# Optimization experiments

Hardware: AMD Instinct MI355X
Metric: run time of the kernel (lower is better)

Reference implementation:

```python
import jax, jax.numpy as jnp
import numpy as np

L, D_IN, D_OUT, H = 4096, 512, 256, 4
HEAD = D_OUT // H  # 64


def setup_inputs() -> dict:
    key = jax.random.key(0)
    k1, k2, k3, k4, k5 = jax.random.split(key, 5)
    h = jax.random.normal(k1, (L, D_IN), dtype=jnp.float32)
    A = jax.random.randint(k2, (L, L), 0, 2, dtype=jnp.int32)
    W = jax.random.normal(k3, (D_OUT, D_IN), dtype=jnp.float32) * 0.05
    attn = jax.random.normal(k4, (H, 2 * HEAD), dtype=jnp.float32) * 0.05
    out_w = jax.random.normal(k5, (D_OUT, D_OUT), dtype=jnp.float32) * 0.05
    out_b = jnp.zeros((D_OUT,), dtype=jnp.float32)
    return {"h": h, "A": A, "W": W, "attn": attn, "out_w": out_w, "out_b": out_b}


def reference(h, A, W, attn, out_w, out_b):
    # h: (L, D_in), A: (L, L) in {0,1}
    Lq = h.shape[0]
    n_heads, two_d = attn.shape
    d = two_d // 2
    Wh = (h @ W.T).reshape(Lq, n_heads, d)  # (L, H, d)
    # Algebraic rewrite of concat-score: e_ij = a1.Wh_i + a2.Wh_j
    a1, a2 = attn[:, :d], attn[:, d:]
    s_i = jnp.einsum("lhd,hd->lh", Wh, a1)  # (L, H)
    s_j = jnp.einsum("lhd,hd->lh", Wh, a2)  # (L, H)
    e = jax.nn.leaky_relu(s_i[:, None, :] + s_j[None, :, :], negative_slope=0.2)  # (L, L, H)
    mask = (A > 0)[:, :, None]  # (L, L, 1)
    NEG = jnp.asarray(-1e30, e.dtype)
    e = jnp.where(mask, e, NEG)
    # stable masked softmax over j (axis=1); rows with no neighbors -> alpha = 0
    m = jnp.max(e, axis=1, keepdims=True)
    m = jnp.where(m > NEG / 2, m, 0.0)
    ex = jnp.where(mask, jnp.exp(e - m), 0.0)
    denom = jnp.sum(ex, axis=1, keepdims=True)
    alpha = ex / jnp.where(denom > 0, denom, 1.0)  # (L, L, H)
    # dropout is identity in eval mode
    out = jnp.einsum("ijh,jhd->ihd", alpha, Wh).reshape(Lq, n_heads * d)
    return out @ out_w.T + out_b
```

## Files before the change

kernel.cpp:

```cpp
#include <hip/hip_runtime.h>
#include <hip/hip_bf16.h>

#define L_    4096
#define DIN   512
#define DOUT  256
#define NH    4
#define HD    64
#define JW    128

typedef unsigned short u16;
typedef __attribute__((ext_vector_type(8))) short short8;
typedef __attribute__((ext_vector_type(4))) float floatx4;

__device__ __forceinline__ float bf2f(u16 u) {
  union { unsigned u32; float f; } v; v.u32 = ((unsigned)u) << 16; return v.f;
}
__device__ __forceinline__ u16 f2bf(float f) {
  union { float f; unsigned u; } v; v.f = f;
  unsigned r = v.u + 0x7fff + ((v.u >> 16) & 1);
  return (u16)(r >> 16);
}
__device__ __forceinline__ unsigned cvt2(float a, float b) {
  __hip_bfloat162 v = __float22bfloat162_rn(make_float2(a, b));
  return *reinterpret_cast<unsigned*>(&v);
}
__device__ __forceinline__ short8 pack8(const float* __restrict__ p) {
  float4 a = *(const float4*)p, b = *(const float4*)(p + 4);
  union { unsigned u[4]; short8 s; } r;
  r.u[0] = cvt2(a.x, a.y); r.u[1] = cvt2(a.z, a.w);
  r.u[2] = cvt2(b.x, b.y); r.u[3] = cvt2(b.z, b.w);
  return r.s;
}

__device__ __forceinline__ void mfma_cdmap(int lane, int* rowm, int* colm) {
  const int c0 = lane & 15;
  union { u16 u[8]; short8 s; } a1, b1, a2, b2;
  const u16 one = f2bf(1.f), cid = f2bf((float)c0);
  #pragma unroll
  for (int j = 0; j < 8; ++j) { a1.u[j] = cid; b1.u[j] = one; a2.u[j] = one; b2.u[j] = cid; }
  floatx4 z = {0.f, 0.f, 0.f, 0.f};
  floatx4 dr = __builtin_amdgcn_mfma_f32_16x16x32_bf16(a1.s, b1.s, z, 0, 0, 0);
  floatx4 dc = __builtin_amdgcn_mfma_f32_16x16x32_bf16(a2.s, b2.s, z, 0, 0, 0);
  #pragma unroll
  for (int r = 0; r < 4; ++r) {
    rowm[r] = (int)(dr[r] * 0.03125f + 0.5f);
    colm[r] = (int)(dc[r] * 0.03125f + 0.5f);
  }
}

__global__ __launch_bounds__(256) void k_ab(const int* __restrict__ A,
                                            unsigned* __restrict__ Abits) {
  const int g = blockIdx.x * 256 + threadIdx.x;
  const int lane = threadIdx.x & 63;
  #pragma unroll
  for (int r = 0; r < 8; ++r) {
    const size_t gi = (size_t)r * 524288 + g;
    int4 v = *(const int4*)(A + gi * 4);
    unsigned nib = (v.x > 0 ? 1u : 0u) | (v.y > 0 ? 2u : 0u)
                 | (v.z > 0 ? 4u : 0u) | (v.w > 0 ? 8u : 0u);
    unsigned part = nib << ((lane & 7) * 4);
    part |= __shfl_xor(part, 1, 64);
    part |= __shfl_xor(part, 2, 64);
    part |= __shfl_xor(part, 4, 64);
    if ((lane & 7) == 0) Abits[gi >> 3] = part;
  }
}

__global__ __launch_bounds__(256) void k0b_wf(const float* __restrict__ W,
                                              u16* __restrict__ Wf) {
  const int g = blockIdx.x * 256 + threadIdx.x;
  const int col = g >> 4, kblock = g & 15;
  const int cg = col >> 6, nt = (col >> 4) & 3, c0 = col & 15;
  const float* src = W + (size_t)col * DIN + kblock * 32;
  u16* dst = Wf + ((size_t)(cg * 4 + nt) * 16 + kblock) * 512 + c0 * 8;
  #pragma unroll
  for (int q = 0; q < 4; ++q) {
    short8 v = pack8(src + q * 8);
    *(short8*)(dst + q * 128) = v;
  }
}

__global__ __launch_bounds__(1024) void k1_wh(
    const float* __restrict__ h, const u16* __restrict__ Wf,
    const float* __restrict__ attn,
    u16* __restrict__ WhTf, float* __restrict__ s1g, float2* __restrict__ bdg)
{
  const int i0 = blockIdx.x * 16;
  const int t = threadIdx.x;
  const int wv = t >> 6, lane = t & 63, q = lane >> 4, c0 = lane & 15;
  const int cg = wv & 3, kc = wv >> 2;
  int rowm[4], colm[4];
  mfma_cdmap(lane, rowm, colm);

  __shared__ u16  hT[16][DIN + 8];
  __shared__ float pA[16][DOUT + 8];
  __shared__ float pB[16][DOUT + 8];
  __shared__ float attnL[NH * 128];

  if (t < 512) attnL[t] = attn[t];
  {
    const int row = t >> 6, c8 = (t & 63) * 8;
    const float* hp = h + (size_t)(i0 + row) * DIN + c8;
    float4 a = *(const float4*)hp;
    float4 b = *(const float4*)(hp + 4);
    union { unsigned u[4]; int4 v; } pk;
    pk.u[0] = cvt2(a.x, a.y); pk.u[1] = cvt2(a.z, a.w);
    pk.u[2] = cvt2(b.x, b.y); pk.u[3] = cvt2(b.z, b.w);
    *(int4*)&hT[row][c8] = pk.v;
  }
  __syncthreads();

  floatx4 acc[4] = {};
  #pragma unroll
  for (int ktl = 0; ktl < 4; ++ktl) {
    const int kb = kc * 128 + ktl * 32 + q * 8;
    short8 af = *(const short8*)&hT[c0][kb];
    #pragma unroll
    for (int nt = 0; nt < 4; ++nt) {
      short8 bf = *(const short8*)(Wf + ((size_t)(cg * 4 + nt) * 16 + kc * 4 + ktl) * 512 + lane * 8);
      acc[nt] = __builtin_amdgcn_mfma_f32_16x16x32_bf16(af, bf, acc[nt], 0, 0, 0);
    }
  }

  auto writeT = [&](float (*P)[DOUT + 8]) {
    #pragma unroll
    for (int nt = 0; nt < 4; ++nt)
      #pragma unroll
      for (int r = 0; r < 4; ++r)
        P[rowm[r]][cg * 64 + nt * 16 + colm[r]] = acc[nt][r];
  };
  auto addB2A = [&]() {
    const int row = t >> 6, c4 = (t & 63) * 4;
    float4* a = (float4*)&pA[row][c4];
    float4 bv = *(float4*)&pB[row][c4];
    float4 av = *a;
    av.x += bv.x; av.y += bv.y; av.z += bv.z; av.w += bv.w;
    *a = av;
  };

  if (kc == 0) writeT(pA);
  if (kc == 1) writeT(pB);
  __syncthreads();
  addB2A();
  __syncthreads();
  if (kc == 2) writeT(pB);
  __syncthreads();
  addB2A();
  __syncthreads();
  if (kc == 3) writeT(pB);
  __syncthreads();
  addB2A();
  __syncthreads();

  if (t < 64) {
    const int r = t & 15, hh = t >> 4;
    float s1 = 0.f, s2 = 0.f;
    for (int d = 0; d < HD; ++d) {
      float v = pA[r][hh * 64 + d];
      s1 += v * attnL[hh * 128 + d];
      s2 += v * attnL[hh * 128 + 64 + d];
    }
    s1g[hh * L_ + i0 + r] = s1;
    bdg[hh * L_ + i0 + r] = make_float2(__expf(s2), __expf(0.2f * s2));
  }

  if (t < 256) {
    const int d = t;
    const int hd = d >> 6, nt = (d >> 4) & 3, dc0 = d & 15;
    const int jblock = i0 >> 5, qbase = (i0 & 31) >> 3;
    u16* base = WhTf + ((size_t)(hd * 4 + nt) * JW + jblock) * 512 + dc0 * 8;
    #pragma unroll
    for (int jh = 0; jh < 2; ++jh) {
      const int i = jh * 8;
      union { unsigned u[4]; int4 v; } pk;
      pk.u[0] = cvt2(pA[i + 0][d], pA[i + 1][d]);
      pk.u[1] = cvt2(pA[i + 2][d], pA[i + 3][d]);
      pk.u[2] = cvt2(pA[i + 4][d], pA[i + 5][d]);
      pk.u[3] = cvt2(pA[i + 6][d], pA[i + 7][d]);
      *(int4*)(base + (qbase + jh) * 128) = pk.v;
    }
  }
}

__global__ __launch_bounds__(1024) void k2_attn(
    const unsigned* __restrict__ Abits, const u16* __restrict__ WhTf,
    const float* __restrict__ s1g, const float2* __restrict__ bdg,
    const float* __restrict__ out_w, const float* __restrict__ out_b,
    float* __restrict__ out)
{
  const int i0 = blockIdx.x * 16;
  const int t = threadIdx.x;
  const int wv = t >> 6, lane = t & 63, q = lane >> 4, c0 = lane & 15;
  const int hd = wv & 3, jc = wv >> 2;

  __shared__ float pA[NH][16][HD + 4];
  __shared__ float pB[NH][16][HD + 4];
  __shared__ float dden[NH][4][16];
  __shared__ float rcpS[NH][16];
  __shared__ u16  CnL[16][DOUT + 8];
  __shared__ unsigned AbitL[16][JW + 2];

  {
    const int row = t >> 6, l = t & 63;
    uint2 w2 = *(const uint2*)&Abits[(size_t)(i0 + row) * JW + l * 2];
    AbitL[row][l * 2] = w2.x;
    AbitL[row][l * 2 + 1] = w2.y;
  }
  int rowm[4], colm[4];
  mfma_cdmap(lane, rowm, colm);
  __syncthreads();

  const float s1v = s1g[hd * L_ + i0 + c0];
  const float av = __expf(s1v);
  const float cv = __expf(0.2f * s1v);
  const float th = __expf(-s1v);
  const float2* bdh = bdg + (size_t)hd * L_;
  const u16* Wc = WhTf + (size_t)(hd * 4) * JW * 512 + (size_t)(jc * 32) * 512 + lane * 8;
  const int jbase = jc * 1024;

  floatx4 acc[4] = {};
  float dpart = 0.f;

  union PF { unsigned u[4]; short8 s; };

  auto issueV = [&](int kt, float4* v) {
    const float2* p = bdh + jbase + kt * 32 + q * 8;
    v[0] = *(const float4*)p;       v[1] = *(const float4*)(p + 2);
    v[2] = *(const float4*)(p + 4); v[3] = *(const float4*)(p + 6);
  };
  auto issueW = [&](int kt, short8* w) {
    #pragma unroll
    for (int nt = 0; nt < 4; ++nt)
      w[nt] = *(const short8*)(Wc + ((size_t)nt * JW + kt) * 512);
  };
  auto sm8 = [&](const float4* v, int kt, PF& pf) {
    const unsigned mb = (AbitL[c0][jc * 32 + kt] >> (q * 8)) & 0xffu;
    const float bb[8] = {v[0].x, v[0].z, v[1].x, v[1].z, v[2].x, v[2].z, v[3].x, v[3].z};
    const float dd[8] = {v[0].y, v[0].w, v[1].y, v[1].w, v[2].y, v[2].w, v[3].y, v[3].w};
    float ex[8];
    #pragma unroll
    for (int jj = 0; jj < 8; ++jj) {
      float p = (bb[jj] >= th) ? (av * bb[jj]) : (cv * dd[jj]);
      ex[jj] = ((mb >> jj) & 1u) ? p : 0.f;
      dpart += ex[jj];
    }
    pf.u[0] = cvt2(ex[0], ex[1]); pf.u[1] = cvt2(ex[2], ex[3]);
    pf.u[2] = cvt2(ex[4], ex[5]); pf.u[3] = cvt2(ex[6], ex[7]);
  };
  auto mfma4 = [&](PF& pf, const short8* w) {
    #pragma unroll
    for (int nt = 0; nt < 4; ++nt)
      acc[nt] = __builtin_amdgcn_mfma_f32_16x16x32_bf16(pf.s, w[nt], acc[nt], 0, 0, 0);
  };

  float4 vA[4], vB[4];
  short8 wA[4], wB[4];
  PF pfA, pfB;

  issueV(0, vA); issueW(0, wA);
  issueV(1, vB); issueW(1, wB);
  __builtin_amdgcn_sched_barrier(0);
  sm8(vA, 0, pfA);

  #pragma unroll 1
  for (int u = 0; u < 15; ++u) {
    const int kt = 2 * u;
    issueV(kt + 2, vA);
    __builtin_amdgcn_sched_barrier(0);
    sm8(vB, kt + 1, pfB);
    mfma4(pfA, wA);
    __builtin_amdgcn_sched_barrier(0);
    issueW(kt + 2, wA);
    issueV(kt + 3, vB);
    __builtin_amdgcn_sched_barrier(0);
    mfma4(pfB, wB);
    __builtin_amdgcn_sched_barrier(0);
    issueW(kt + 3, wB);
    sm8(vA, kt + 2, pfA);
    __builtin_amdgcn_sched_barrier(0);
  }
  mfma4(pfA, wA);
  sm8(vB, 31, pfB);
  mfma4(pfB, wB);

  dpart += __shfl_xor(dpart, 16, 64);
  dpart += __shfl_xor(dpart, 32, 64);
  if (lane < 16) dden[hd][jc][lane] = dpart;

  auto writeT = [&](float (*P)[HD + 4]) {
    #pragma unroll
    for (int nt = 0; nt < 4; ++nt)
      #pragma unroll
      for (int r = 0; r < 4; ++r)
        P[rowm[r]][nt * 16 + colm[r]] = acc[nt][r];
  };
  auto addB2A = [&]() {
    const int h2 = t >> 8, rem = t & 255, row = rem >> 4, d4 = (rem & 15) * 4;
    float4* a = (float4*)&pA[h2][row][d4];
    float4 bv = *(float4*)&pB[h2][row][d4];
    float4 av2 = *a;
    av2.x += bv.x; av2.y += bv.y; av2.z += bv.z; av2.w += bv.w;
    *a = av2;
  };

  if (jc == 0) writeT(pA[hd]);
  if (jc == 1) writeT(pB[hd]);
  __syncthreads();
  if (t < 64) {
    const int hh = t >> 4, r = t & 15;
    float den = dden[hh][0][r] + dden[hh][1][r] + dden[hh][2][r] + dden[hh][3][r];
    rcpS[hh][r] = (den > 0.f) ? (1.f / den) : 0.f;
  }
  addB2A();
  __syncthreads();
  if (jc == 2) writeT(pB[hd]);
  __syncthreads();
  addB2A();
  __syncthreads();
  if (jc == 3) writeT(pB[hd]);
  __syncthreads();
  addB2A();
  __syncthreads();

  {
    const int row = t >> 6, c4 = (t & 63) * 4;
    #pragma unroll
    for (int x = 0; x < 4; ++x) {
      const int col = c4 + x;
      const int hh = col >> 6, d = col & 63;
      CnL[row][col] = f2bf(pA[hh][row][d] * rcpS[hh][row]);
    }
  }
  __syncthreads();

  if (wv < 4) {
    const int cg = wv;
    floatx4 o[4] = {};
    #pragma unroll
    for (int kt = 0; kt < DOUT / 32; ++kt) {
      const int kb2 = kt * 32 + q * 8;
      short8 afr = *(const short8*)(&CnL[c0][kb2]);
      #pragma unroll
      for (int nt = 0; nt < 4; ++nt) {
        const int col = cg * 64 + nt * 16 + c0;
        short8 bfo = pack8(out_w + (size_t)col * DOUT + kb2);
        o[nt] = __builtin_amdgcn_mfma_f32_16x16x32_bf16(afr, bfo, o[nt], 0, 0, 0);
      }
    }
    #pragma unroll
    for (int nt = 0; nt < 4; ++nt)
      #pragma unroll
      for (int r = 0; r < 4; ++r) {
        const int col = cg * 64 + nt * 16 + colm[r];
        out[(size_t)(i0 + rowm[r]) * DOUT + col] = o[nt][r] + out_b[col];
      }
  }
}

extern "C" void kernel_launch(void* const* d_in, const int* in_sizes, int n_in,
                              void* d_out, int out_size, void* d_ws, size_t ws_size,
                              hipStream_t stream) {
  const float* h     = (const float*)d_in[0];
  const int*   A     = (const int*)d_in[1];
  const float* W     = (const float*)d_in[2];
  const float* attn  = (const float*)d_in[3];
  const float* out_w = (const float*)d_in[4];
  const float* out_b = (const float*)d_in[5];
  float* outp = (float*)d_out;

  const size_t WHTF_B = (size_t)DOUT * L_ * 2;
  const size_t S1_B   = (size_t)NH * L_ * 4;
  const size_t BD_B   = (size_t)NH * L_ * 8;
  const size_t AB_OFF = WHTF_B + S1_B + BD_B;
  u16*    WhTf = (u16*)d_ws;
  float*  s1g  = (float*)((char*)d_ws + WHTF_B);
  float2* bdg  = (float2*)((char*)d_ws + WHTF_B + S1_B);
  unsigned* Abits = (ws_size >= AB_OFF + (size_t)L_ * JW * 4 )
                  ? (unsigned*)((char*)d_ws + AB_OFF)
                  : (unsigned*)((char*)d_out + 2097152);
  u16* Wf = (u16*)d_out;

  hipLaunchKernelGGL(k_ab, dim3(2048), dim3(256), 0, stream, A, Abits);
  hipLaunchKernelGGL(k0b_wf, dim3(16), dim3(256), 0, stream, W, Wf);
  hipLaunchKernelGGL(k1_wh, dim3(L_ / 16), dim3(1024), 0, stream,
                     h, Wf, attn, WhTf, s1g, bdg);
  hipLaunchKernelGGL(k2_attn, dim3(L_ / 16), dim3(1024), 0, stream,
                     Abits, WhTf, s1g, bdg, out_w, out_b, outp);
}
```

Baseline: 156.3 us.

## Fuse adjacency bit-packing into Wh kernel and split attention loop into two accumulators

The separate adjacency bit-packing kernel becomes a set of extra blocks in the Wh projection kernel, so the A-to-bits conversion runs alongside the projection and one launch is removed. The attention kernel's hand-pipelined, sched_barrier-driven double-buffer loop is replaced by a simpler loop that handles two independent k-tiles per iteration with separate accumulators, which are summed at the end. This depends on the compiler for load/compute overlap and uses more registers. Block 0 work and bitpacking now share the same launch.

```diff
diff --git a/kernel.cpp b/kernel.cpp
--- a/kernel.cpp
+++ b/kernel.cpp
@@ -45,24 +45,6 @@
   for (int r = 0; r < 4; ++r) {
     rowm[r] = (int)(dr[r] * 0.03125f + 0.5f);
     colm[r] = (int)(dc[r] * 0.03125f + 0.5f);
-  }
-}
-
-__global__ __launch_bounds__(256) void k_ab(const int* __restrict__ A,
-                                            unsigned* __restrict__ Abits) {
-  const int g = blockIdx.x * 256 + threadIdx.x;
-  const int lane = threadIdx.x & 63;
-  #pragma unroll
-  for (int r = 0; r < 8; ++r) {
-    const size_t gi = (size_t)r * 524288 + g;
-    int4 v = *(const int4*)(A + gi * 4);
-    unsigned nib = (v.x > 0 ? 1u : 0u) | (v.y > 0 ? 2u : 0u)
-                 | (v.z > 0 ? 4u : 0u) | (v.w > 0 ? 8u : 0u);
-    unsigned part = nib << ((lane & 7) * 4);
-    part |= __shfl_xor(part, 1, 64);
-    part |= __shfl_xor(part, 2, 64);
-    part |= __shfl_xor(part, 4, 64);
-    if ((lane & 7) == 0) Abits[gi >> 3] = part;
   }
 }
 
@@ -80,13 +62,34 @@
   }
 }
 
-__global__ __launch_bounds__(1024) void k1_wh(
+__global__ __launch_bounds__(1024) void k1f(
     const float* __restrict__ h, const u16* __restrict__ Wf,
     const float* __restrict__ attn,
-    u16* __restrict__ WhTf, float* __restrict__ s1g, float2* __restrict__ bdg)
+    u16* __restrict__ WhTf, float* __restrict__ s1g, float2* __restrict__ bdg,
+    const int* __restrict__ A, unsigned* __restrict__ Abits)
 {
+  const int t = threadIdx.x;
+
+  if (blockIdx.x >= 256) {
+    const int bid2 = blockIdx.x - 256;
+    const int g = bid2 * 1024 + t;
+    const int lane = t & 63;
+    #pragma unroll
+    for (int r = 0; r < 8; ++r) {
+      const size_t gi = (size_t)r * 524288 + g;
+      int4 v = *(const int4*)(A + gi * 4);
+      unsigned nib = (v.x > 0 ? 1u : 0u) | (v.y > 0 ? 2u : 0u)
+                   | (v.z > 0 ? 4u : 0u) | (v.w > 0 ? 8u : 0u);
+      unsigned part = nib << ((lane & 7) * 4);
+      part |= __shfl_xor(part, 1, 64);
+      part |= __shfl_xor(part, 2, 64);
+      part |= __shfl_xor(part, 4, 64);
+      if ((lane & 7) == 0) Abits[gi >> 3] = part;
+    }
+    return;
+  }
+
   const int i0 = blockIdx.x * 16;
-  const int t = threadIdx.x;
   const int wv = t >> 6, lane = t & 63, q = lane >> 4, c0 = lane & 15;
   const int cg = wv & 3, kc = wv >> 2;
   int rowm[4], colm[4];
@@ -218,23 +221,13 @@
   const u16* Wc = WhTf + (size_t)(hd * 4) * JW * 512 + (size_t)(jc * 32) * 512 + lane * 8;
   const int jbase = jc * 1024;
 
-  floatx4 acc[4] = {};
-  float dpart = 0.f;
-
   union PF { unsigned u[4]; short8 s; };
 
-  auto issueV = [&](int kt, float4* v) {
-    const float2* p = bdh + jbase + kt * 32 + q * 8;
-    v[0] = *(const float4*)p;       v[1] = *(const float4*)(p + 2);
-    v[2] = *(const float4*)(p + 4); v[3] = *(const float4*)(p + 6);
-  };
-  auto issueW = [&](int kt, short8* w) {
-    #pragma unroll
-    for (int nt = 0; nt < 4; ++nt)
-      w[nt] = *(const short8*)(Wc + ((size_t)nt * JW + kt) * 512);
-  };
-  auto sm8 = [&](const float4* v, int kt, PF& pf) {
-    const unsigned mb = (AbitL[c0][jc * 32 + kt] >> (q * 8)) & 0xffu;
+  floatx4 accA[4] = {}, accB[4] = {};
+  float dpA = 0.f, dpB = 0.f;
+
+  auto sm8 = [&](const float4* v, unsigned mword, float& dp) -> PF {
+    const unsigned mb = (mword >> (q * 8)) & 0xffu;
     const float bb[8] = {v[0].x, v[0].z, v[1].x, v[1].z, v[2].x, v[2].z, v[3].x, v[3].z};
     const float dd[8] = {v[0].y, v[0].w, v[1].y, v[1].w, v[2].y, v[2].w, v[3].y, v[3].w};
     float ex[8];
@@ -242,46 +235,46 @@
     for (int jj = 0; jj < 8; ++jj) {
       float p = (bb[jj] >= th) ? (av * bb[jj]) : (cv * dd[jj]);
       ex[jj] = ((mb >> jj) & 1u) ? p : 0.f;
-      dpart += ex[jj];
-    }
+      dp += ex[jj];
+    }
+    PF pf;
     pf.u[0] = cvt2(ex[0], ex[1]); pf.u[1] = cvt2(ex[2], ex[3]);
     pf.u[2] = cvt2(ex[4], ex[5]); pf.u[3] = cvt2(ex[6], ex[7]);
-  };
-  auto mfma4 = [&](PF& pf, const short8* w) {
-    #pragma unroll
-    for (int nt = 0; nt < 4; ++nt)
-      acc[nt] = __builtin_amdgcn_mfma_f32_16x16x32_bf16(pf.s, w[nt], acc[nt], 0, 0, 0);
-  };
-
-  float4 vA[4], vB[4];
-  short8 wA[4], wB[4];
-  PF pfA, pfB;
-
-  issueV(0, vA); issueW(0, wA);
-  issueV(1, vB); issueW(1, wB);
-  __builtin_amdgcn_sched_barrier(0);
-  sm8(vA, 0, pfA);
+    return pf;
+  };
 
   #pragma unroll 1
-  for (int u = 0; u < 15; ++u) {
-    const int kt = 2 * u;
-    issueV(kt + 2, vA);
-    __builtin_amdgcn_sched_barrier(0);
-    sm8(vB, kt + 1, pfB);
-    mfma4(pfA, wA);
-    __builtin_amdgcn_sched_barrier(0);
-    issueW(kt + 2, wA);
-    issueV(kt + 3, vB);
-    __builtin_amdgcn_sched_barrier(0);
-    mfma4(pfB, wB);
-    __builtin_amdgcn_sched_barrier(0);
-    issueW(kt + 3, wB);
-    sm8(vA, kt + 2, pfA);
-    __builtin_amdgcn_sched_barrier(0);
-  }
-  mfma4(pfA, wA);
-  sm8(vB, 31, pfB);
-  mfma4(pfB, wB);
+  for (int kt = 0; kt < 16; ++kt) {
+    const int ka = kt, kb = kt + 16;
+    const float2* pa = bdh + jbase + ka * 32 + q * 8;
+    const float2* pb = bdh + jbase + kb * 32 + q * 8;
+    float4 va[4], vb[4];
+    va[0] = *(const float4*)pa;       va[1] = *(const float4*)(pa + 2);
+    va[2] = *(const float4*)(pa + 4); va[3] = *(const float4*)(pa + 6);
+    vb[0] = *(const float4*)pb;       vb[1] = *(const float4*)(pb + 2);
+    vb[2] = *(const float4*)(pb + 4); vb[3] = *(const float4*)(pb + 6);
+    short8 wa[4], wb[4];
+    #pragma unroll
+    for (int nt = 0; nt < 4; ++nt) {
+      wa[nt] = *(const short8*)(Wc + ((size_t)nt * JW + ka) * 512);
+      wb[nt] = *(const short8*)(Wc + ((size_t)nt * JW + kb) * 512);
+    }
+    const unsigned mwa = AbitL[c0][jc * 32 + ka];
+    const unsigned mwb = AbitL[c0][jc * 32 + kb];
+    PF pfa = sm8(va, mwa, dpA);
+    #pragma unroll
+    for (int nt = 0; nt < 4; ++nt)
+      accA[nt] = __builtin_amdgcn_mfma_f32_16x16x32_bf16(pfa.s, wa[nt], accA[nt], 0, 0, 0);
+    PF pfb = sm8(vb, mwb, dpB);
+    #pragma unroll
+    for (int nt = 0; nt < 4; ++nt)
+      accB[nt] = __builtin_amdgcn_mfma_f32_16x16x32_bf16(pfb.s, wb[nt], accB[nt], 0, 0, 0);
+  }
+
+  floatx4 acc[4];
+  #pragma unroll
+  for (int nt = 0; nt < 4; ++nt) acc[nt] = accA[nt] + accB[nt];
+  float dpart = dpA + dpB;
 
   dpart += __shfl_xor(dpart, 16, 64);
   dpart += __shfl_xor(dpart, 32, 64);
@@ -375,15 +368,14 @@
   u16*    WhTf = (u16*)d_ws;
   float*  s1g  = (float*)((char*)d_ws + WHTF_B);
   float2* bdg  = (float2*)((char*)d_ws + WHTF_B + S1_B);
-  unsigned* Abits = (ws_size >= AB_OFF + (size_t)L_ * JW * 4 )
+  unsigned* Abits = (ws_size >= AB_OFF + (size_t)L_ * JW * 4)
                   ? (unsigned*)((char*)d_ws + AB_OFF)
                   : (unsigned*)((char*)d_out + 2097152);
   u16* Wf = (u16*)d_out;
 
-  hipLaunchKernelGGL(k_ab, dim3(2048), dim3(256), 0, stream, A, Abits);
   hipLaunchKernelGGL(k0b_wf, dim3(16), dim3(256), 0, stream, W, Wf);
-  hipLaunchKernelGGL(k1_wh, dim3(L_ / 16), dim3(1024), 0, stream,
-                     h, Wf, attn, WhTf, s1g, bdg);
+  hipLaunchKernelGGL(k1f, dim3(768), dim3(1024), 0, stream,
+                     h, Wf, attn, WhTf, s1g, bdg, A, Abits);
   hipLaunchKernelGGL(k2_attn, dim3(L_ / 16), dim3(1024), 0, stream,
                      Abits, WhTf, s1g, bdg, out_w, out_b, outp);
 }
```

Measured after the change: 164.9 us. 1.05x slower.

## Split attention j-range across two blocks with flag-based partial reduction

Applied to the files above, without the earlier changes.

Each 16-row tile's neighbour range is split across two blocks, doubling the grid of the attention kernel to fill more CUs. The first block to finish writes its unnormalised partial numerator and denominator to workspace, and the second block spins on a flag, merges them and applies the output projection. The W repack kernel is folded into the adjacency bitpacking kernel to drop one launch, and the hand-pipelined software prefetch loop is replaced by a simple loop. This adds a global round trip, spin-waiting and a dependence on workspace size, and it loses the explicit load/compute overlap.

```diff
diff --git a/kernel.cpp b/kernel.cpp
--- a/kernel.cpp
+++ b/kernel.cpp
@@ -49,9 +49,13 @@
 }
 
 __global__ __launch_bounds__(256) void k_ab(const int* __restrict__ A,
-                                            unsigned* __restrict__ Abits) {
-  const int g = blockIdx.x * 256 + threadIdx.x;
-  const int lane = threadIdx.x & 63;
+                                            unsigned* __restrict__ Abits,
+                                            const float* __restrict__ W,
+                                            u16* __restrict__ Wf,
+                                            int* flags) {
+  const int t = threadIdx.x;
+  const int g = blockIdx.x * 256 + t;
+  const int lane = t & 63;
   #pragma unroll
   for (int r = 0; r < 8; ++r) {
     const size_t gi = (size_t)r * 524288 + g;
@@ -64,19 +68,17 @@
     part |= __shfl_xor(part, 4, 64);
     if ((lane & 7) == 0) Abits[gi >> 3] = part;
   }
-}
-
-__global__ __launch_bounds__(256) void k0b_wf(const float* __restrict__ W,
-                                              u16* __restrict__ Wf) {
-  const int g = blockIdx.x * 256 + threadIdx.x;
-  const int col = g >> 4, kblock = g & 15;
-  const int cg = col >> 6, nt = (col >> 4) & 3, c0 = col & 15;
-  const float* src = W + (size_t)col * DIN + kblock * 32;
-  u16* dst = Wf + ((size_t)(cg * 4 + nt) * 16 + kblock) * 512 + c0 * 8;
-  #pragma unroll
-  for (int q = 0; q < 4; ++q) {
-    short8 v = pack8(src + q * 8);
-    *(short8*)(dst + q * 128) = v;
+  if (flags && blockIdx.x == 0) { flags[t] = 0; flags[t + 256] = 0; }
+  if (blockIdx.x < 16) {
+    const int col = g >> 4, kblock = g & 15;
+    const int cg = col >> 6, nt = (col >> 4) & 3, c0 = col & 15;
+    const float* src = W + (size_t)col * DIN + kblock * 32;
+    u16* dst = Wf + ((size_t)(cg * 4 + nt) * 16 + kblock) * 512 + c0 * 8;
+    #pragma unroll
+    for (int q = 0; q < 4; ++q) {
+      short8 v = pack8(src + q * 8);
+      *(short8*)(dst + q * 128) = v;
+    }
   }
 }
 
@@ -182,13 +184,20 @@
   }
 }
 
-__global__ __launch_bounds__(1024) void k2_attn(
+template<int JS>
+__global__ __launch_bounds__(1024, (JS == 2 ? 8 : 4)) void k2_attn(
     const unsigned* __restrict__ Abits, const u16* __restrict__ WhTf,
     const float* __restrict__ s1g, const float2* __restrict__ bdg,
     const float* __restrict__ out_w, const float* __restrict__ out_b,
-    float* __restrict__ out)
+    float* __restrict__ out,
+    float* __restrict__ partNum, float* __restrict__ partDen, int* flags)
 {
-  const int i0 = blockIdx.x * 16;
+  constexpr int JWH = JW / JS;
+  constexpr int KT  = 32 / JS;
+  const int bid = blockIdx.x;
+  const int jh   = (JS == 2) ? (bid & 1) : 0;
+  const int tile = (JS == 2) ? (bid >> 1) : bid;
+  const int i0 = tile * 16;
   const int t = threadIdx.x;
   const int wv = t >> 6, lane = t & 63, q = lane >> 4, c0 = lane & 15;
   const int hd = wv & 3, jc = wv >> 2;
@@ -198,13 +207,18 @@
   __shared__ float dden[NH][4][16];
   __shared__ float rcpS[NH][16];
   __shared__ u16  CnL[16][DOUT + 8];
-  __shared__ unsigned AbitL[16][JW + 2];
+  __shared__ unsigned AbitL[16][JWH + 2];
+  __shared__ int oldv;
 
   {
     const int row = t >> 6, l = t & 63;
-    uint2 w2 = *(const uint2*)&Abits[(size_t)(i0 + row) * JW + l * 2];
-    AbitL[row][l * 2] = w2.x;
-    AbitL[row][l * 2 + 1] = w2.y;
+    if (JS == 1) {
+      uint2 w2 = *(const uint2*)&Abits[(size_t)(i0 + row) * JW + l * 2];
+      AbitL[row][l * 2] = w2.x;
+      AbitL[row][l * 2 + 1] = w2.y;
+    } else {
+      AbitL[row][l] = Abits[(size_t)(i0 + row) * JW + jh * JWH + l];
+    }
   }
   int rowm[4], colm[4];
   mfma_cdmap(lane, rowm, colm);
@@ -214,74 +228,40 @@
   const float av = __expf(s1v);
   const float cv = __expf(0.2f * s1v);
   const float th = __expf(-s1v);
-  const float2* bdh = bdg + (size_t)hd * L_;
-  const u16* Wc = WhTf + (size_t)(hd * 4) * JW * 512 + (size_t)(jc * 32) * 512 + lane * 8;
-  const int jbase = jc * 1024;
-
+  const int jblk0 = jh * JWH;
+  const float2* bdh = bdg + (size_t)hd * L_ + jblk0 * 32 + jc * (1024 / JS);
+  const u16* Wc = WhTf + ((size_t)(hd * 4) * JW + jblk0 + jc * KT) * 512 + lane * 8;
+
+  union PF { unsigned u[4]; short8 s; };
   floatx4 acc[4] = {};
   float dpart = 0.f;
 
-  union PF { unsigned u[4]; short8 s; };
-
-  auto issueV = [&](int kt, float4* v) {
-    const float2* p = bdh + jbase + kt * 32 + q * 8;
-    v[0] = *(const float4*)p;       v[1] = *(const float4*)(p + 2);
-    v[2] = *(const float4*)(p + 4); v[3] = *(const float4*)(p + 6);
-  };
-  auto issueW = [&](int kt, short8* w) {
+  #pragma unroll 1
+  for (int kt = 0; kt < KT; ++kt) {
+    const float2* p = bdh + kt * 32 + q * 8;
+    float4 v0 = *(const float4*)p;       float4 v1 = *(const float4*)(p + 2);
+    float4 v2 = *(const float4*)(p + 4); float4 v3 = *(const float4*)(p + 6);
+    short8 w[4];
     #pragma unroll
     for (int nt = 0; nt < 4; ++nt)
       w[nt] = *(const short8*)(Wc + ((size_t)nt * JW + kt) * 512);
-  };
-  auto sm8 = [&](const float4* v, int kt, PF& pf) {
-    const unsigned mb = (AbitL[c0][jc * 32 + kt] >> (q * 8)) & 0xffu;
-    const float bb[8] = {v[0].x, v[0].z, v[1].x, v[1].z, v[2].x, v[2].z, v[3].x, v[3].z};
-    const float dd[8] = {v[0].y, v[0].w, v[1].y, v[1].w, v[2].y, v[2].w, v[3].y, v[3].w};
+    const unsigned mb = (AbitL[c0][jc * KT + kt] >> (q * 8)) & 0xffu;
+    const float bb[8] = {v0.x, v0.z, v1.x, v1.z, v2.x, v2.z, v3.x, v3.z};
+    const float dd[8] = {v0.y, v0.w, v1.y, v1.w, v2.y, v2.w, v3.y, v3.w};
     float ex[8];
     #pragma unroll
     for (int jj = 0; jj < 8; ++jj) {
-      float p = (bb[jj] >= th) ? (av * bb[jj]) : (cv * dd[jj]);
-      ex[jj] = ((mb >> jj) & 1u) ? p : 0.f;
+      float pp = (bb[jj] >= th) ? (av * bb[jj]) : (cv * dd[jj]);
+      ex[jj] = ((mb >> jj) & 1u) ? pp : 0.f;
       dpart += ex[jj];
     }
+    PF pf;
     pf.u[0] = cvt2(ex[0], ex[1]); pf.u[1] = cvt2(ex[2], ex[3]);
     pf.u[2] = cvt2(ex[4], ex[5]); pf.u[3] = cvt2(ex[6], ex[7]);
-  };
-  auto mfma4 = [&](PF& pf, const short8* w) {
     #pragma unroll
     for (int nt = 0; nt < 4; ++nt)
       acc[nt] = __builtin_amdgcn_mfma_f32_16x16x32_bf16(pf.s, w[nt], acc[nt], 0, 0, 0);
-  };
-
-  float4 vA[4], vB[4];
-  short8 wA[4], wB[4];
-  PF pfA, pfB;
-
-  issueV(0, vA); issueW(0, wA);
-  issueV(1, vB); issueW(1, wB);
-  __builtin_amdgcn_sched_barrier(0);
-  sm8(vA, 0, pfA);
-
-  #pragma unroll 1
-  for (int u = 0; u < 15; ++u) {
-    const int kt = 2 * u;
-    issueV(kt + 2, vA);
-    __builtin_amdgcn_sched_barrier(0);
-    sm8(vB, kt + 1, pfB);
-    mfma4(pfA, wA);
-    __builtin_amdgcn_sched_barrier(0);
-    issueW(kt + 2, wA);
-    issueV(kt + 3, vB);
-    __builtin_amdgcn_sched_barrier(0);
-    mfma4(pfB, wB);
-    __builtin_amdgcn_sched_barrier(0);
-    issueW(kt + 3, wB);
-    sm8(vA, kt + 2, pfA);
-    __builtin_amdgcn_sched_barrier(0);
-  }
-  mfma4(pfA, wA);
-  sm8(vB, 31, pfB);
-  mfma4(pfB, wB);
+  }
 
   dpart += __shfl_xor(dpart, 16, 64);
   dpart += __shfl_xor(dpart, 32, 64);
@@ -309,7 +289,7 @@
   if (t < 64) {
     const int hh = t >> 4, r = t & 15;
     float den = dden[hh][0][r] + dden[hh][1][r] + dden[hh][2][r] + dden[hh][3][r];
-    rcpS[hh][r] = (den > 0.f) ? (1.f / den) : 0.f;
+    rcpS[hh][r] = (JS == 1) ? ((den > 0.f) ? (1.f / den) : 0.f) : den;
   }
   addB2A();
   __syncthreads();
@@ -321,6 +301,43 @@
   __syncthreads();
   addB2A();
   __syncthreads();
+
+  if (JS == 2) {
+    if (t == 0)
+      oldv = __hip_atomic_fetch_add(&flags[tile], 1, __ATOMIC_ACQ_REL,
+                                    __HIP_MEMORY_SCOPE_AGENT);
+    __syncthreads();
+    const int row = t >> 6, c4 = (t & 63) * 4;
+    const int hh = c4 >> 6, d = c4 & 63;
+    float* pslot = partNum + ((size_t)tile * 16 + row) * 256 + c4;
+    if (oldv == 0) {
+      *(float4*)pslot = *(const float4*)&pA[hh][row][d];
+      if (t < 64) partDen[tile * 64 + t] = rcpS[t >> 4][t & 15];
+      __syncthreads();
+      if (t == 0)
+        __hip_atomic_store(&flags[256 + tile], 1, __ATOMIC_RELEASE,
+                           __HIP_MEMORY_SCOPE_AGENT);
+      return;
+    }
+    if (t == 0) {
+      while (__hip_atomic_load(&flags[256 + tile], __ATOMIC_ACQUIRE,
+                               __HIP_MEMORY_SCOPE_AGENT) == 0)
+        __builtin_amdgcn_s_sleep(1);
+    }
+    __syncthreads();
+    {
+      float4 o = *(const float4*)pslot;
+      float4* a = (float4*)&pA[hh][row][d];
+      float4 av2 = *a;
+      av2.x += o.x; av2.y += o.y; av2.z += o.z; av2.w += o.w;
+      *a = av2;
+    }
+    if (t < 64) {
+      float den = rcpS[t >> 4][t & 15] + partDen[tile * 64 + t];
+      rcpS[t >> 4][t & 15] = (den > 0.f) ? (1.f / den) : 0.f;
+    }
+    __syncthreads();
+  }
 
   {
     const int row = t >> 6, c4 = (t & 63) * 4;
@@ -368,22 +385,40 @@
   const float* out_b = (const float*)d_in[5];
   float* outp = (float*)d_out;
 
-  const size_t WHTF_B = (size_t)DOUT * L_ * 2;
-  const size_t S1_B   = (size_t)NH * L_ * 4;
-  const size_t BD_B   = (size_t)NH * L_ * 8;
-  const size_t AB_OFF = WHTF_B + S1_B + BD_B;
+  const size_t WHTF_B  = (size_t)DOUT * L_ * 2;
+  const size_t S1_B    = (size_t)NH * L_ * 4;
+  const size_t BD_B    = (size_t)NH * L_ * 8;
+  const size_t ABITS_B = (size_t)L_ * JW * 4;
+  const size_t AB_OFF  = WHTF_B + S1_B + BD_B;
+  const size_t PN_OFF  = AB_OFF + ABITS_B;
+  const size_t PN_B    = (size_t)256 * 16 * 256 * 4;
+  const size_t PD_B    = (size_t)256 * 64 * 4;
+  const size_t FL_B    = 512 * 4;
+  const size_t TOTAL   = PN_OFF + PN_B + PD_B + FL_B;
+
   u16*    WhTf = (u16*)d_ws;
   float*  s1g  = (float*)((char*)d_ws + WHTF_B);
   float2* bdg  = (float2*)((char*)d_ws + WHTF_B + S1_B);
-  unsigned* Abits = (ws_size >= AB_OFF + (size_t)L_ * JW * 4 )
+  const bool split = (ws_size >= TOTAL);
+  unsigned* Abits = (ws_size >= PN_OFF)
                   ? (unsigned*)((char*)d_ws + AB_OFF)
                   : (unsigned*)((char*)d_out + 2097152);
+  float* partNum = (float*)((char*)d_ws + PN_OFF);
+  float* partDen = (float*)((char*)d_ws + PN_OFF + PN_B);
+  int*   flags   = (int*)((char*)d_ws + PN_OFF + PN_B + PD_B);
   u16* Wf = (u16*)d_out;
 
-  hipLaunchKernelGGL(k_ab, dim3(2048), dim3(256), 0, stream, A, Abits);
-  hipLaunchKernelGGL(k0b_wf, dim3(16), dim3(256), 0, stream, W, Wf);
+  hipLaunchKernelGGL(k_ab, dim3(2048), dim3(256), 0, stream,
+                     A, Abits, W, Wf, split ? flags : (int*)nullptr);
   hipLaunchKernelGGL(k1_wh, dim3(L_ / 16), dim3(1024), 0, stream,
                      h, Wf, attn, WhTf, s1g, bdg);
-  hipLaunchKernelGGL(k2_attn, dim3(L_ / 16), dim3(1024), 0, stream,
-                     Abits, WhTf, s1g, bdg, out_w, out_b, outp);
-}
+  if (split) {
+    hipLaunchKernelGGL((k2_attn<2>), dim3(L_ / 16 * 2), dim3(1024), 0, stream,
+                       Abits, WhTf, s1g, bdg, out_w, out_b, outp,
+                       partNum, partDen, flags);
+  } else {
+    hipLaunchKernelGGL((k2_attn<1>), dim3(L_ / 16), dim3(1024), 0, stream,
+                       Abits, WhTf, s1g, bdg, out_w, out_b, outp,
+                       partNum, partDen, flags);
+  }
+}
```

Result: slower. 184.6 us (+18.1%).

## Fold W repack into A-bitpack kernel and drop split-K in projection kernel

Applied to the files above, without the earlier changes.

Merges the small W-to-bf16 repack kernel into the adjacency bit-packing kernel (first 16 blocks do it), removing one launch. The h@W^T projection kernel changes from 1024 threads with 4-way split-K and a serialized shared-memory reduction to 256 threads where each wave does the full K loop. The attention score dot products are split across all threads with a small shared reduction. This trades fewer barriers and less shared memory for less parallelism per block and a longer serial MFMA chain per wave.

```diff
diff --git a/kernel.cpp b/kernel.cpp
--- a/kernel.cpp
+++ b/kernel.cpp
@@ -49,9 +49,12 @@
 }
 
 __global__ __launch_bounds__(256) void k_ab(const int* __restrict__ A,
-                                            unsigned* __restrict__ Abits) {
-  const int g = blockIdx.x * 256 + threadIdx.x;
-  const int lane = threadIdx.x & 63;
+                                            unsigned* __restrict__ Abits,
+                                            const float* __restrict__ W,
+                                            u16* __restrict__ Wf) {
+  const int t = threadIdx.x;
+  const int g = blockIdx.x * 256 + t;
+  const int lane = t & 63;
   #pragma unroll
   for (int r = 0; r < 8; ++r) {
     const size_t gi = (size_t)r * 524288 + g;
@@ -64,23 +67,20 @@
     part |= __shfl_xor(part, 4, 64);
     if ((lane & 7) == 0) Abits[gi >> 3] = part;
   }
-}
-
-__global__ __launch_bounds__(256) void k0b_wf(const float* __restrict__ W,
-                                              u16* __restrict__ Wf) {
-  const int g = blockIdx.x * 256 + threadIdx.x;
-  const int col = g >> 4, kblock = g & 15;
-  const int cg = col >> 6, nt = (col >> 4) & 3, c0 = col & 15;
-  const float* src = W + (size_t)col * DIN + kblock * 32;
-  u16* dst = Wf + ((size_t)(cg * 4 + nt) * 16 + kblock) * 512 + c0 * 8;
-  #pragma unroll
-  for (int q = 0; q < 4; ++q) {
-    short8 v = pack8(src + q * 8);
-    *(short8*)(dst + q * 128) = v;
-  }
-}
-
-__global__ __launch_bounds__(1024) void k1_wh(
+  if (blockIdx.x < 16) {
+    const int col = g >> 4, kblock = g & 15;
+    const int cg = col >> 6, nt = (col >> 4) & 3, c0 = col & 15;
+    const float* src = W + (size_t)col * DIN + kblock * 32;
+    u16* dst = Wf + ((size_t)(cg * 4 + nt) * 16 + kblock) * 512 + c0 * 8;
+    #pragma unroll
+    for (int q = 0; q < 4; ++q) {
+      short8 v = pack8(src + q * 8);
+      *(short8*)(dst + q * 128) = v;
+    }
+  }
+}
+
+__global__ __launch_bounds__(256) void k1_wh(
     const float* __restrict__ h, const u16* __restrict__ Wf,
     const float* __restrict__ attn,
     u16* __restrict__ WhTf, float* __restrict__ s1g, float2* __restrict__ bdg)
@@ -88,18 +88,22 @@
   const int i0 = blockIdx.x * 16;
   const int t = threadIdx.x;
   const int wv = t >> 6, lane = t & 63, q = lane >> 4, c0 = lane & 15;
-  const int cg = wv & 3, kc = wv >> 2;
+  const int cg = wv;
   int rowm[4], colm[4];
   mfma_cdmap(lane, rowm, colm);
 
   __shared__ u16  hT[16][DIN + 8];
   __shared__ float pA[16][DOUT + 8];
-  __shared__ float pB[16][DOUT + 8];
   __shared__ float attnL[NH * 128];
-
-  if (t < 512) attnL[t] = attn[t];
-  {
-    const int row = t >> 6, c8 = (t & 63) * 8;
+  __shared__ float s1p[4][64];
+  __shared__ float s2p[4][64];
+
+  attnL[t] = attn[t];
+  attnL[t + 256] = attn[t + 256];
+  #pragma unroll
+  for (int rep = 0; rep < 4; ++rep) {
+    const int idx = rep * 256 + t;
+    const int row = idx >> 6, c8 = (idx & 63) * 8;
     const float* hp = h + (size_t)(i0 + row) * DIN + c8;
     float4 a = *(const float4*)hp;
     float4 b = *(const float4*)(hp + 4);
@@ -112,59 +116,46 @@
 
   floatx4 acc[4] = {};
   #pragma unroll
-  for (int ktl = 0; ktl < 4; ++ktl) {
-    const int kb = kc * 128 + ktl * 32 + q * 8;
+  for (int ks = 0; ks < 16; ++ks) {
+    const int kb = ks * 32 + q * 8;
     short8 af = *(const short8*)&hT[c0][kb];
     #pragma unroll
     for (int nt = 0; nt < 4; ++nt) {
-      short8 bf = *(const short8*)(Wf + ((size_t)(cg * 4 + nt) * 16 + kc * 4 + ktl) * 512 + lane * 8);
+      short8 bf = *(const short8*)(Wf + ((size_t)(cg * 4 + nt) * 16 + ks) * 512 + lane * 8);
       acc[nt] = __builtin_amdgcn_mfma_f32_16x16x32_bf16(af, bf, acc[nt], 0, 0, 0);
     }
   }
 
-  auto writeT = [&](float (*P)[DOUT + 8]) {
-    #pragma unroll
-    for (int nt = 0; nt < 4; ++nt)
-      #pragma unroll
-      for (int r = 0; r < 4; ++r)
-        P[rowm[r]][cg * 64 + nt * 16 + colm[r]] = acc[nt][r];
-  };
-  auto addB2A = [&]() {
-    const int row = t >> 6, c4 = (t & 63) * 4;
-    float4* a = (float4*)&pA[row][c4];
-    float4 bv = *(float4*)&pB[row][c4];
-    float4 av = *a;
-    av.x += bv.x; av.y += bv.y; av.z += bv.z; av.w += bv.w;
-    *a = av;
-  };
-
-  if (kc == 0) writeT(pA);
-  if (kc == 1) writeT(pB);
-  __syncthreads();
-  addB2A();
-  __syncthreads();
-  if (kc == 2) writeT(pB);
-  __syncthreads();
-  addB2A();
-  __syncthreads();
-  if (kc == 3) writeT(pB);
-  __syncthreads();
-  addB2A();
-  __syncthreads();
-
-  if (t < 64) {
-    const int r = t & 15, hh = t >> 4;
+  #pragma unroll
+  for (int nt = 0; nt < 4; ++nt)
+    #pragma unroll
+    for (int r = 0; r < 4; ++r)
+      pA[rowm[r]][cg * 64 + nt * 16 + colm[r]] = acc[nt][r];
+  __syncthreads();
+
+  {
+    const int r = t & 15, hh = (t >> 4) & 3, qt = t >> 6;
     float s1 = 0.f, s2 = 0.f;
-    for (int d = 0; d < HD; ++d) {
+    #pragma unroll
+    for (int dd = 0; dd < 16; ++dd) {
+      const int d = qt * 16 + dd;
       float v = pA[r][hh * 64 + d];
       s1 += v * attnL[hh * 128 + d];
       s2 += v * attnL[hh * 128 + 64 + d];
     }
+    s1p[qt][hh * 16 + r] = s1;
+    s2p[qt][hh * 16 + r] = s2;
+  }
+  __syncthreads();
+  if (t < 64) {
+    const int r = t & 15, hh = t >> 4;
+    float s1 = s1p[0][t] + s1p[1][t] + s1p[2][t] + s1p[3][t];
+    float s2 = s2p[0][t] + s2p[1][t] + s2p[2][t] + s2p[3][t];
     s1g[hh * L_ + i0 + r] = s1;
     bdg[hh * L_ + i0 + r] = make_float2(__expf(s2), __expf(0.2f * s2));
   }
 
-  if (t < 256) {
+  {
     const int d = t;
     const int hd = d >> 6, nt = (d >> 4) & 3, dc0 = d & 15;
     const int jblock = i0 >> 5, qbase = (i0 & 31) >> 3;
@@ -368,21 +359,22 @@
   const float* out_b = (const float*)d_in[5];
   float* outp = (float*)d_out;
 
-  const size_t WHTF_B = (size_t)DOUT * L_ * 2;
-  const size_t S1_B   = (size_t)NH * L_ * 4;
-  const size_t BD_B   = (size_t)NH * L_ * 8;
-  const size_t AB_OFF = WHTF_B + S1_B + BD_B;
+  const size_t WHTF_B  = (size_t)DOUT * L_ * 2;
+  const size_t S1_B    = (size_t)NH * L_ * 4;
+  const size_t BD_B    = (size_t)NH * L_ * 8;
+  const size_t ABITS_B = (size_t)L_ * JW * 4;
+  const size_t AB_OFF  = WHTF_B + S1_B + BD_B;
+
   u16*    WhTf = (u16*)d_ws;
   float*  s1g  = (float*)((char*)d_ws + WHTF_B);
   float2* bdg  = (float2*)((char*)d_ws + WHTF_B + S1_B);
-  unsigned* Abits = (ws_size >= AB_OFF + (size_t)L_ * JW * 4 )
+  unsigned* Abits = (ws_size >= AB_OFF + ABITS_B)
                   ? (unsigned*)((char*)d_ws + AB_OFF)
                   : (unsigned*)((char*)d_out + 2097152);
   u16* Wf = (u16*)d_out;
 
-  hipLaunchKernelGGL(k_ab, dim3(2048), dim3(256), 0, stream, A, Abits);
-  hipLaunchKernelGGL(k0b_wf, dim3(16), dim3(256), 0, stream, W, Wf);
-  hipLaunchKernelGGL(k1_wh, dim3(L_ / 16), dim3(1024), 0, stream,
+  hipLaunchKernelGGL(k_ab, dim3(2048), dim3(256), 0, stream, A, Abits, W, Wf);
+  hipLaunchKernelGGL(k1_wh, dim3(L_ / 16), dim3(256), 0, stream,
                      h, Wf, attn, WhTf, s1g, bdg);
   hipLaunchKernelGGL(k2_attn, dim3(L_ / 16), dim3(1024), 0, stream,
                      Abits, WhTf, s1g, bdg, out_w, out_b, outp);
```

After: 153.7 us. Within noise of the previous version (-1.7%).
